# Kernel optimization log

Hardware: AMD Instinct MI355X
Metric: run time of the kernel (lower is better)

Reference implementation:

```python
import jax, jax.numpy as jnp
import numpy as np

CHEB_K = 3  # diffusion_steps

def setup_inputs() -> dict:
    key = jax.random.key(0)
    k1, k2, k3 = jax.random.split(key, 3)
    N, D, B, C, O, K = 2048, 16, 64, 64, 64, CHEB_K
    node_embeddings = jax.random.normal(k1, (N, D), dtype=jnp.float32)
    feat = jax.random.normal(k2, (B, N, C), dtype=jnp.float32)
    # kaiming-uniform-like init for weights_pool, zeros bias (matches reset_parameters)
    fan_in = K * C  # fan_in of [D, K, C, O] per torch convention (dims after first)
    bound = 1.0 / np.sqrt(fan_in)
    weights_pool = jax.random.uniform(k3, (D, K, C, O), dtype=jnp.float32,
                                      minval=-bound, maxval=bound)
    bias_pool = jnp.zeros((D, O), dtype=jnp.float32)
    return {"node_embeddings": node_embeddings, "feat": feat,
            "weights_pool": weights_pool, "bias_pool": bias_pool}

def reference(node_embeddings, feat, weights_pool, bias_pool):
    N = node_embeddings.shape[0]
    K = weights_pool.shape[1]
    # adaptive adjacency: softmax(relu(E E^T)) row-wise
    sim = node_embeddings @ node_embeddings.T            # [N, N]
    supports = jax.nn.softmax(jax.nn.relu(sim), axis=1)  # [N, N]
    # Chebyshev polynomial recurrence: T0=I, T1=A, Tk = 2A Tk-1 - Tk-2
    support_set = [jnp.eye(N, dtype=supports.dtype), supports]
    for _ in range(2, K):
        support_set.append(2.0 * supports @ support_set[-1] - support_set[-2])
    supports_k = jnp.stack(support_set, axis=0)          # [K, N, N]
    # node-conditioned weights and bias
    weights = jnp.einsum('nd,dkio->nkio', node_embeddings, weights_pool)  # [N,K,C,O]
    bias = node_embeddings @ bias_pool                                    # [N, O]
    # graph diffusion of features
    x_g = jnp.einsum('knm,bmc->bknc', supports_k, feat)  # [B, K, N, C]
    x_g = jnp.transpose(x_g, (0, 2, 1, 3))               # [B, N, K, C]
    # per-node batched GEMM + bias
    x_gconv = jnp.einsum('bnki,nkio->bno', x_g, weights) + bias
    return x_gconv
```

## Files before the change

kernel.cpp:

```cpp
#include <hip/hip_runtime.h>
#include <stdint.h>

#define NN 2048
#define DE 16
#define BB 64
#define CC 64
#define OO 64
#define BC 4096
#define KR 192
#define JJ 12288

using bf16x8 = __attribute__((ext_vector_type(8))) __bf16;
using f32x4  = __attribute__((ext_vector_type(4))) float;

__device__ __forceinline__ unsigned short f2bf(float f) {
  union { float f; unsigned int u; } v; v.f = f;
  unsigned int u = v.u;
  return (unsigned short)((u + 0x7FFFu + ((u >> 16) & 1u)) >> 16);
}
__device__ __forceinline__ float bf2f(unsigned short h) {
  union { unsigned int u; float f; } v; v.u = ((unsigned int)h) << 16;
  return v.f;
}
__device__ __forceinline__ void gll16(const void* g, void* l) {
  __builtin_amdgcn_global_load_lds(
      (const __attribute__((address_space(1))) unsigned int*)g,
      (__attribute__((address_space(3))) unsigned int*)l, 16, 0, 0);
}

__global__ __launch_bounds__(256) void prep(const float* __restrict__ feat,
                                            const float* __restrict__ E,
                                            const float* __restrict__ wp,
                                            const float* __restrict__ bp,
                                            unsigned short* __restrict__ Fbf,
                                            unsigned short* __restrict__ FbfT,
                                            unsigned short* __restrict__ Abf,
                                            float* __restrict__ Bias,
                                            unsigned short* __restrict__ Ebf,
                                            unsigned short* __restrict__ wpT2) {
  __shared__ float smem[64 * 65];
  const int id = blockIdx.x;
  const int t  = threadIdx.x;

  if (id < 2048) {
    float (*tile)[65] = (float (*)[65])smem;
    const int b  = id >> 5;
    const int n0 = (id & 31) * 64;
    const int tr = t >> 4, tc4 = (t & 15) * 4;
#pragma unroll
    for (int i = 0; i < 4; ++i) {
      const int r = tr + i * 16;
      const float4 v = *(const float4*)(feat + (size_t)b * (NN * CC) + (size_t)(n0 + r) * CC + tc4);
      tile[r][tc4 + 0] = v.x; tile[r][tc4 + 1] = v.y;
      tile[r][tc4 + 2] = v.z; tile[r][tc4 + 3] = v.w;
    }
    __syncthreads();
#pragma unroll
    for (int i = 0; i < 4; ++i) {
      const int r = tr + i * 16;
      const unsigned int lo = f2bf(tile[r][tc4 + 0]) | ((unsigned int)f2bf(tile[r][tc4 + 1]) << 16);
      const unsigned int hi = f2bf(tile[r][tc4 + 2]) | ((unsigned int)f2bf(tile[r][tc4 + 3]) << 16);
      *(uint2*)(Fbf + (size_t)(n0 + r) * BC + b * CC + tc4) = make_uint2(lo, hi);
    }
    const int rr = t & 63;
    const int cb = t >> 6;
#pragma unroll
    for (int i = 0; i < 16; ++i) {
      const int c = cb * 16 + i;
      FbfT[(size_t)(b * CC + c) * NN + n0 + rr] = f2bf(tile[rr][c]);
    }
  } else if (id < 4096) {
    const int n = id - 2048;
    float* en  = smem;
    float* red = smem + 16;
    if (t < 16) en[t] = E[n * 16 + t];
    __syncthreads();
    if (t < 16) Ebf[n * 16 + t] = f2bf(en[t]);
    float er[16];
#pragma unroll
    for (int d = 0; d < 16; ++d) er[d] = en[d];

    float v[8];
    float mx = 0.0f;
#pragma unroll
    for (int i = 0; i < 8; ++i) {
      const int m = t + i * 256;
      const float4* Em = (const float4*)(E + m * 16);
      const float4 a = Em[0], b = Em[1], c = Em[2], d = Em[3];
      float dot = er[0] * a.x + er[1] * a.y + er[2] * a.z + er[3] * a.w
                + er[4] * b.x + er[5] * b.y + er[6] * b.z + er[7] * b.w
                + er[8] * c.x + er[9] * c.y + er[10] * c.z + er[11] * c.w
                + er[12] * d.x + er[13] * d.y + er[14] * d.z + er[15] * d.w;
      v[i] = fmaxf(dot, 0.0f);
      mx = fmaxf(mx, v[i]);
    }
#pragma unroll
    for (int off = 32; off > 0; off >>= 1) mx = fmaxf(mx, __shfl_xor(mx, off, 64));
    const int wave = t >> 6, lane = t & 63;
    if (lane == 0) red[wave] = mx;
    __syncthreads();
    mx = fmaxf(fmaxf(red[0], red[1]), fmaxf(red[2], red[3]));
    float s = 0.0f;
#pragma unroll
    for (int i = 0; i < 8; ++i) { v[i] = __expf(v[i] - mx); s += v[i]; }
#pragma unroll
    for (int off = 32; off > 0; off >>= 1) s += __shfl_xor(s, off, 64);
    if (lane == 0) red[4 + wave] = s;
    __syncthreads();
    s = red[4] + red[5] + red[6] + red[7];
    const float inv = 1.0f / s;
#pragma unroll
    for (int i = 0; i < 8; ++i)
      Abf[(size_t)n * NN + t + i * 256] = f2bf(v[i] * inv);
    if (t < 64) {
      float bs = 0.0f;
#pragma unroll
      for (int d = 0; d < 16; ++d) bs += er[d] * bp[d * 64 + t];
      Bias[n * 64 + t] = bs;
    }
  } else {
    const int rq = id - 4096;
    for (int p = t; p < 1024; p += 256) {
      const int e0 = p * 8;
      const int d0 = e0 & 15;
      const int rem = e0 >> 4;
      const int rl = rem & 7, o = rem >> 3;
      const int r = rq * 8 + rl;
      unsigned int w[4];
#pragma unroll
      for (int u = 0; u < 4; ++u) {
        const float f0 = wp[(size_t)(d0 + 2 * u) * JJ + r * 64 + o];
        const float f1 = wp[(size_t)(d0 + 2 * u + 1) * JJ + r * 64 + o];
        w[u] = f2bf(f0) | ((unsigned int)f2bf(f1) << 16);
      }
      *(uint4*)(wpT2 + (size_t)rq * 8192 + e0) = make_uint4(w[0], w[1], w[2], w[3]);
    }
  }
}

__global__ __launch_bounds__(256) void make_w_mfma(const unsigned short* __restrict__ Ebf,
                                                   const unsigned short* __restrict__ wpT2,
                                                   unsigned short* __restrict__ Wg) {
  __shared__ alignas(16) unsigned short As[128 * 16];
  __shared__ alignas(16) unsigned short Bs[128 * 16];
  const int t = threadIdx.x;
  const int bm = blockIdx.y * 128;
  const int bj = blockIdx.x * 128;
  gll16(Ebf  + (size_t)(bm + (t >> 1)) * 16 + (t & 1) * 8, &As[t * 8]);
  gll16(wpT2 + (size_t)(bj + (t >> 1)) * 16 + (t & 1) * 8, &Bs[t * 8]);
  __syncthreads();
  const int wave = t >> 6, lane = t & 63;
  const int wm = (wave >> 1) * 64, wj = (wave & 1) * 64;
  const int li = lane & 15, q = lane >> 4;
  const bool hiK = (q >= 2);
  const int qq = q & 1;
  bf16x8 vz;
#pragma unroll
  for (int i = 0; i < 8; ++i) vz[i] = (__bf16)0.0f;

  bf16x8 af[4], bfr[4];
#pragma unroll
  for (int r = 0; r < 4; ++r) {
    af[r] = *(const bf16x8*)&As[(wm + r * 16 + li) * 16 + qq * 8];
    if (hiK) af[r] = vz;
  }
#pragma unroll
  for (int c = 0; c < 4; ++c) {
    bfr[c] = *(const bf16x8*)&Bs[(wj + c * 16 + li) * 16 + qq * 8];
    if (hiK) bfr[c] = vz;
  }
  const int rowL = q * 4;
#pragma unroll
  for (int r = 0; r < 4; ++r) {
#pragma unroll
    for (int c = 0; c < 4; ++c) {
      f32x4 acc = (f32x4){0.f, 0.f, 0.f, 0.f};
      acc = __builtin_amdgcn_mfma_f32_16x16x32_bf16(af[r], bfr[c], acc, 0, 0, 0);
      const int gm = bm + wm + r * 16 + rowL;
      const int gj = bj + wj + c * 16 + li;
#pragma unroll
      for (int i = 0; i < 4; ++i)
        Wg[(size_t)(gm + i) * JJ + gj] = f2bf(acc[i]);
    }
  }
}

template <int EPI>
__global__ __launch_bounds__(256, 2) void gemm128(const unsigned short* __restrict__ A,
                                                  const unsigned short* __restrict__ Bt,
                                                  unsigned short* __restrict__ Cnm,
                                                  unsigned short* __restrict__ Ct,
                                                  const unsigned short* __restrict__ F) {
  __shared__ alignas(16) unsigned short As[128 * 64];
  __shared__ alignas(16) unsigned short Bs[128 * 64];
  const int t = threadIdx.x;
  const int bm = blockIdx.y * 128, bn = blockIdx.x * 128;
  const int wave = t >> 6, lane = t & 63;
  const int wm = (wave >> 1) * 64, wn = (wave & 1) * 64;

  f32x4 acc[4][4];
#pragma unroll
  for (int r = 0; r < 4; ++r)
#pragma unroll
    for (int c = 0; c < 4; ++c) acc[r][c] = (f32x4){0.f, 0.f, 0.f, 0.f};

  const int srow = t >> 3;
  const int csw = (((t & 7) ^ ((t >> 4) & 7)) * 8);
  const unsigned short* Ap[4];
  const unsigned short* Bp[4];
#pragma unroll
  for (int i = 0; i < 4; ++i) {
    Ap[i] = A  + (size_t)(bm + srow + i * 32) * NN + csw;
    Bp[i] = Bt + (size_t)(bn + srow + i * 32) * NN + csw;
  }
  const int li = lane & 15, q = lane >> 4, sw = (li >> 1) & 7;
  const int arow = (wm + li) * 64, brow = (wn + li) * 64;

  for (int k0 = 0; k0 < NN; k0 += 64) {
    __syncthreads();
#pragma unroll
    for (int i = 0; i < 4; ++i) gll16(Ap[i] + k0, &As[(t + i * 256) * 8]);
#pragma unroll
    for (int i = 0; i < 4; ++i) gll16(Bp[i] + k0, &Bs[(t + i * 256) * 8]);
    __syncthreads();
#pragma unroll
    for (int kk = 0; kk < 2; ++kk) {
      bf16x8 af[4], bfr[4];
#pragma unroll
      for (int r = 0; r < 4; ++r)
        af[r] = *(const bf16x8*)&As[arow + r * 16 * 64 + (((kk * 4 + q) ^ sw) * 8)];
#pragma unroll
      for (int c = 0; c < 4; ++c)
        bfr[c] = *(const bf16x8*)&Bs[brow + c * 16 * 64 + (((kk * 4 + q) ^ sw) * 8)];
#pragma unroll
      for (int r = 0; r < 4; ++r)
#pragma unroll
        for (int c = 0; c < 4; ++c)
          acc[r][c] = __builtin_amdgcn_mfma_f32_16x16x32_bf16(af[r], bfr[c], acc[r][c], 0, 0, 0);
    }
  }

  const int colL = lane & 15, rowL = (lane >> 4) * 4;
#pragma unroll
  for (int r = 0; r < 4; ++r) {
#pragma unroll
    for (int c = 0; c < 4; ++c) {
      const int gm = bm + wm + r * 16 + rowL;
      const int gn = bn + wn + c * 16 + colL;
      const f32x4 a = acc[r][c];
      if (EPI == 1) {
#pragma unroll
        for (int i = 0; i < 4; ++i)
          Cnm[(size_t)(gm + i) * BC + gn] = f2bf(a[i]);
        const unsigned int lo = f2bf(a[0]) | ((unsigned int)f2bf(a[1]) << 16);
        const unsigned int hi = f2bf(a[2]) | ((unsigned int)f2bf(a[3]) << 16);
        *(uint2*)(Ct + (size_t)gn * NN + gm) = make_uint2(lo, hi);
      } else {
#pragma unroll
        for (int i = 0; i < 4; ++i) {
          const float g = 2.0f * a[i] - bf2f(F[(size_t)(gm + i) * BC + gn]);
          Cnm[(size_t)(gm + i) * BC + gn] = f2bf(g);
        }
      }
    }
  }
}

__global__ __launch_bounds__(256) void final_gemm(const unsigned short* __restrict__ Fbf,
                                                  const unsigned short* __restrict__ G1,
                                                  const unsigned short* __restrict__ G2,
                                                  const unsigned short* __restrict__ Wg,
                                                  const float* __restrict__ Bias,
                                                  float* __restrict__ out) {
  __shared__ alignas(16) unsigned short Xl[64 * 200];
  __shared__ alignas(16) unsigned short Wl[KR * OO];
  const int n = blockIdx.x, t = threadIdx.x;
  const unsigned short* srcs[3] = {Fbf + (size_t)n * BC, G1 + (size_t)n * BC, G2 + (size_t)n * BC};
#pragma unroll
  for (int kk = 0; kk < 3; ++kk) {
    const uint4* s = (const uint4*)srcs[kk];
    for (int p = t; p < 512; p += 256) {
      const uint4 v = s[p];
      const int j = p * 8, b = j >> 6, i = j & 63;
      *(uint4*)&Xl[b * 200 + kk * 64 + i] = v;
    }
  }
  {
    const uint4* s = (const uint4*)(Wg + (size_t)n * JJ);
    uint4* d = (uint4*)Wl;
    for (int p = t; p < 1536; p += 256) d[p] = s[p];
  }
  __syncthreads();

  const int wave = t >> 6, lane = t & 63;
  const int q = lane >> 4;
  const int brow = wave * 16 + (lane & 15);
  f32x4 acc[4];
#pragma unroll
  for (int c = 0; c < 4; ++c) acc[c] = (f32x4){0.f, 0.f, 0.f, 0.f};
#pragma unroll
  for (int kq = 0; kq < 6; ++kq) {
    const bf16x8 a = *(const bf16x8*)&Xl[brow * 200 + kq * 32 + q * 8];
#pragma unroll
    for (int c = 0; c < 4; ++c) {
      const bf16x8 b = *(const bf16x8*)&Wl[(kq * 4 + q) * 512 + (c * 16 + (lane & 15)) * 8];
      acc[c] = __builtin_amdgcn_mfma_f32_16x16x32_bf16(a, b, acc[c], 0, 0, 0);
    }
  }
  const int col = lane & 15, rbase = wave * 16 + q * 4;
#pragma unroll
  for (int c = 0; c < 4; ++c) {
    const int o = c * 16 + col;
    const float bs = Bias[n * 64 + o];
#pragma unroll
    for (int i = 0; i < 4; ++i)
      out[(size_t)(rbase + i) * (NN * OO) + (size_t)n * OO + o] = acc[c][i] + bs;
  }
}

extern "C" void kernel_launch(void* const* d_in, const int* in_sizes, int n_in,
                              void* d_out, int out_size, void* d_ws, size_t ws_size,
                              hipStream_t stream) {
  const float* E    = (const float*)d_in[0];
  const float* feat = (const float*)d_in[1];
  const float* wp   = (const float*)d_in[2];
  const float* bp   = (const float*)d_in[3];
  float* out = (float*)d_out;

  char* ws = (char*)d_ws;
  size_t off = 0;
  auto alloc = [&](size_t bytes) -> void* {
    void* p = ws + off;
    off += (bytes + 255) & ~(size_t)255;
    return p;
  };
  unsigned short* Abf  = (unsigned short*)alloc((size_t)NN * NN * 2);
  unsigned short* FbfT = (unsigned short*)alloc((size_t)BC * NN * 2);
  unsigned short* Fbf  = (unsigned short*)alloc((size_t)NN * BC * 2);
  unsigned short* G1   = (unsigned short*)alloc((size_t)NN * BC * 2);
  unsigned short* G1T  = (unsigned short*)alloc((size_t)BC * NN * 2);
  unsigned short* Wg   = (unsigned short*)alloc((size_t)NN * JJ * 2);
  float* Bias          = (float*)alloc((size_t)NN * OO * 4);
  unsigned short* Ebf  = (unsigned short*)alloc((size_t)NN * DE * 2);
  unsigned short* wpT2 = (unsigned short*)alloc((size_t)JJ * DE * 2);
  unsigned short* G2   = FbfT;

  prep<<<dim3(4120), 256, 0, stream>>>(feat, E, wp, bp, Fbf, FbfT, Abf, Bias, Ebf, wpT2);
  make_w_mfma<<<dim3(96, 16), 256, 0, stream>>>(Ebf, wpT2, Wg);
  gemm128<1><<<dim3(32, 16), 256, 0, stream>>>(Abf, FbfT, G1, G1T, nullptr);
  gemm128<2><<<dim3(32, 16), 256, 0, stream>>>(Abf, G1T, G2, nullptr, Fbf);
  final_gemm<<<dim3(2048), 256, 0, stream>>>(Fbf, G1, G2, Wg, Bias, out);
}
```

Baseline: 219.5 us.

## Merge weight-generation into first diffusion GEMM and shrink GEMM tiles to 128x64

Folds the make_w_mfma weight-generation kernel into the first diffusion GEMM launch as extra blocks (ids >= 1024), so the two independent workloads run concurrently and one launch is removed. The diffusion GEMMs switch from 128x128 tiles to 128x64 tiles with each wave computing 32 rows, doubling block count to 1024 and raising the occupancy hint to 4 blocks per CU. This aims to fill the 256 CUs better, at the cost of less data reuse per tile and more global loads of the A operand.

New measurement: 223.8 us. Within noise of the previous version (+1.9%).

```diff
diff --git a/kernel.cpp b/kernel.cpp
--- a/kernel.cpp
+++ b/kernel.cpp
@@ -138,115 +138,114 @@
   }
 }
 
-__global__ __launch_bounds__(256) void make_w_mfma(const unsigned short* __restrict__ Ebf,
-                                                   const unsigned short* __restrict__ wpT2,
-                                                   unsigned short* __restrict__ Wg) {
-  __shared__ alignas(16) unsigned short As[128 * 16];
-  __shared__ alignas(16) unsigned short Bs[128 * 16];
-  const int t = threadIdx.x;
-  const int bm = blockIdx.y * 128;
-  const int bj = blockIdx.x * 128;
-  gll16(Ebf  + (size_t)(bm + (t >> 1)) * 16 + (t & 1) * 8, &As[t * 8]);
-  gll16(wpT2 + (size_t)(bj + (t >> 1)) * 16 + (t & 1) * 8, &Bs[t * 8]);
-  __syncthreads();
-  const int wave = t >> 6, lane = t & 63;
-  const int wm = (wave >> 1) * 64, wj = (wave & 1) * 64;
-  const int li = lane & 15, q = lane >> 4;
-  const bool hiK = (q >= 2);
-  const int qq = q & 1;
-  bf16x8 vz;
-#pragma unroll
-  for (int i = 0; i < 8; ++i) vz[i] = (__bf16)0.0f;
-
-  bf16x8 af[4], bfr[4];
-#pragma unroll
-  for (int r = 0; r < 4; ++r) {
-    af[r] = *(const bf16x8*)&As[(wm + r * 16 + li) * 16 + qq * 8];
-    if (hiK) af[r] = vz;
-  }
-#pragma unroll
-  for (int c = 0; c < 4; ++c) {
-    bfr[c] = *(const bf16x8*)&Bs[(wj + c * 16 + li) * 16 + qq * 8];
-    if (hiK) bfr[c] = vz;
-  }
-  const int rowL = q * 4;
-#pragma unroll
-  for (int r = 0; r < 4; ++r) {
-#pragma unroll
-    for (int c = 0; c < 4; ++c) {
-      f32x4 acc = (f32x4){0.f, 0.f, 0.f, 0.f};
-      acc = __builtin_amdgcn_mfma_f32_16x16x32_bf16(af[r], bfr[c], acc, 0, 0, 0);
-      const int gm = bm + wm + r * 16 + rowL;
-      const int gj = bj + wj + c * 16 + li;
-#pragma unroll
-      for (int i = 0; i < 4; ++i)
-        Wg[(size_t)(gm + i) * JJ + gj] = f2bf(acc[i]);
-    }
-  }
-}
-
-template <int EPI>
-__global__ __launch_bounds__(256, 2) void gemm128(const unsigned short* __restrict__ A,
+template <int EPI, int MW>
+__global__ __launch_bounds__(256, 4) void gemm_mw(const unsigned short* __restrict__ A,
                                                   const unsigned short* __restrict__ Bt,
                                                   unsigned short* __restrict__ Cnm,
                                                   unsigned short* __restrict__ Ct,
-                                                  const unsigned short* __restrict__ F) {
+                                                  const unsigned short* __restrict__ F,
+                                                  const unsigned short* __restrict__ Ebf,
+                                                  const unsigned short* __restrict__ wpT2,
+                                                  unsigned short* __restrict__ Wg) {
   __shared__ alignas(16) unsigned short As[128 * 64];
-  __shared__ alignas(16) unsigned short Bs[128 * 64];
+  __shared__ alignas(16) unsigned short Bs[64 * 64];
+  const int id = blockIdx.x;
   const int t = threadIdx.x;
-  const int bm = blockIdx.y * 128, bn = blockIdx.x * 128;
   const int wave = t >> 6, lane = t & 63;
-  const int wm = (wave >> 1) * 64, wn = (wave & 1) * 64;
-
-  f32x4 acc[4][4];
-#pragma unroll
-  for (int r = 0; r < 4; ++r)
+  const int li = lane & 15, q = lane >> 4;
+
+  if (MW && id >= 1024) {
+    const int wid = id - 1024;
+    const int bj = (wid % 96) * 128;
+    const int bm = (wid / 96) * 128;
+    gll16(Ebf  + (size_t)(bm + (t >> 1)) * 16 + (t & 1) * 8, &As[t * 8]);
+    gll16(wpT2 + (size_t)(bj + (t >> 1)) * 16 + (t & 1) * 8, &Bs[t * 8]);
+    __syncthreads();
+    const int wm = (wave >> 1) * 64, wj = (wave & 1) * 64;
+    const bool hiK = (q >= 2);
+    const int qq = q & 1;
+    bf16x8 vz;
+#pragma unroll
+    for (int i = 0; i < 8; ++i) vz[i] = (__bf16)0.0f;
+    bf16x8 af[4], bfr[4];
+#pragma unroll
+    for (int r = 0; r < 4; ++r) {
+      af[r] = *(const bf16x8*)&As[(wm + r * 16 + li) * 16 + qq * 8];
+      if (hiK) af[r] = vz;
+    }
+#pragma unroll
+    for (int c = 0; c < 4; ++c) {
+      bfr[c] = *(const bf16x8*)&Bs[(wj + c * 16 + li) * 16 + qq * 8];
+      if (hiK) bfr[c] = vz;
+    }
+    const int rowL = q * 4;
+#pragma unroll
+    for (int r = 0; r < 4; ++r) {
+#pragma unroll
+      for (int c = 0; c < 4; ++c) {
+        f32x4 acc = (f32x4){0.f, 0.f, 0.f, 0.f};
+        acc = __builtin_amdgcn_mfma_f32_16x16x32_bf16(af[r], bfr[c], acc, 0, 0, 0);
+        const int gm = bm + wm + r * 16 + rowL;
+        const int gj = bj + wj + c * 16 + li;
+#pragma unroll
+        for (int i = 0; i < 4; ++i)
+          Wg[(size_t)(gm + i) * JJ + gj] = f2bf(acc[i]);
+      }
+    }
+    return;
+  }
+
+  const int bm = (id >> 6) * 128, bn = (id & 63) * 64;
+  const int wm = wave * 32;
+
+  f32x4 acc[2][4];
+#pragma unroll
+  for (int r = 0; r < 2; ++r)
 #pragma unroll
     for (int c = 0; c < 4; ++c) acc[r][c] = (f32x4){0.f, 0.f, 0.f, 0.f};
 
   const int srow = t >> 3;
   const int csw = (((t & 7) ^ ((t >> 4) & 7)) * 8);
   const unsigned short* Ap[4];
-  const unsigned short* Bp[4];
-#pragma unroll
-  for (int i = 0; i < 4; ++i) {
-    Ap[i] = A  + (size_t)(bm + srow + i * 32) * NN + csw;
-    Bp[i] = Bt + (size_t)(bn + srow + i * 32) * NN + csw;
-  }
-  const int li = lane & 15, q = lane >> 4, sw = (li >> 1) & 7;
-  const int arow = (wm + li) * 64, brow = (wn + li) * 64;
+  const unsigned short* Bp[2];
+#pragma unroll
+  for (int i = 0; i < 4; ++i) Ap[i] = A + (size_t)(bm + srow + i * 32) * NN + csw;
+#pragma unroll
+  for (int i = 0; i < 2; ++i) Bp[i] = Bt + (size_t)(bn + srow + i * 32) * NN + csw;
+  const int sw = (li >> 1) & 7;
 
   for (int k0 = 0; k0 < NN; k0 += 64) {
     __syncthreads();
 #pragma unroll
     for (int i = 0; i < 4; ++i) gll16(Ap[i] + k0, &As[(t + i * 256) * 8]);
 #pragma unroll
-    for (int i = 0; i < 4; ++i) gll16(Bp[i] + k0, &Bs[(t + i * 256) * 8]);
+    for (int i = 0; i < 2; ++i) gll16(Bp[i] + k0, &Bs[(t + i * 256) * 8]);
     __syncthreads();
 #pragma unroll
     for (int kk = 0; kk < 2; ++kk) {
-      bf16x8 af[4], bfr[4];
-#pragma unroll
-      for (int r = 0; r < 4; ++r)
-        af[r] = *(const bf16x8*)&As[arow + r * 16 * 64 + (((kk * 4 + q) ^ sw) * 8)];
+      const int kc = ((kk * 4 + q) ^ sw) * 8;
+      bf16x8 af[2], bfr[4];
+#pragma unroll
+      for (int r = 0; r < 2; ++r)
+        af[r] = *(const bf16x8*)&As[(wm + r * 16 + li) * 64 + kc];
 #pragma unroll
       for (int c = 0; c < 4; ++c)
-        bfr[c] = *(const bf16x8*)&Bs[brow + c * 16 * 64 + (((kk * 4 + q) ^ sw) * 8)];
-#pragma unroll
-      for (int r = 0; r < 4; ++r)
+        bfr[c] = *(const bf16x8*)&Bs[(c * 16 + li) * 64 + kc];
+#pragma unroll
+      for (int r = 0; r < 2; ++r)
 #pragma unroll
         for (int c = 0; c < 4; ++c)
           acc[r][c] = __builtin_amdgcn_mfma_f32_16x16x32_bf16(af[r], bfr[c], acc[r][c], 0, 0, 0);
     }
   }
 
-  const int colL = lane & 15, rowL = (lane >> 4) * 4;
-#pragma unroll
-  for (int r = 0; r < 4; ++r) {
+  const int rowL = q * 4;
+#pragma unroll
+  for (int r = 0; r < 2; ++r) {
 #pragma unroll
     for (int c = 0; c < 4; ++c) {
       const int gm = bm + wm + r * 16 + rowL;
-      const int gn = bn + wn + c * 16 + colL;
+      const int gn = bn + c * 16 + li;
       const f32x4 a = acc[r][c];
       if (EPI == 1) {
 #pragma unroll
@@ -346,8 +345,7 @@
   unsigned short* G2   = FbfT;
 
   prep<<<dim3(4120), 256, 0, stream>>>(feat, E, wp, bp, Fbf, FbfT, Abf, Bias, Ebf, wpT2);
-  make_w_mfma<<<dim3(96, 16), 256, 0, stream>>>(Ebf, wpT2, Wg);
-  gemm128<1><<<dim3(32, 16), 256, 0, stream>>>(Abf, FbfT, G1, G1T, nullptr);
-  gemm128<2><<<dim3(32, 16), 256, 0, stream>>>(Abf, G1T, G2, nullptr, Fbf);
+  gemm_mw<1, 1><<<dim3(2560), 256, 0, stream>>>(Abf, FbfT, G1, G1T, nullptr, Ebf, wpT2, Wg);
+  gemm_mw<2, 0><<<dim3(1024), 256, 0, stream>>>(Abf, G1T, G2, nullptr, Fbf, Ebf, wpT2, Wg);
   final_gemm<<<dim3(2048), 256, 0, stream>>>(Fbf, G1, G2, Wg, Bias, out);
 }
```
